# Performance work log

Hardware: AMD Instinct MI355X
Metric: run time of the kernel (lower is better)

Reference implementation:

```python
import jax, jax.numpy as jnp
import numpy as np

# Model hyperparameters (match init_kwargs)
DIM = 512
NUM_HEAD = 8
WS = 2
ALPHA = 0.5
HEAD_DIM = DIM // NUM_HEAD            # 64
L_HEAD = int(NUM_HEAD * ALPHA)        # 4
L_DIM = L_HEAD * HEAD_DIM             # 256
H_HEAD = NUM_HEAD - L_HEAD            # 4
H_DIM = H_HEAD * HEAD_DIM             # 256
SCALE = HEAD_DIM ** (-0.5)


def conv1x1(x, W, b):
    # S_conv treated as pointwise 1x1 conv: channel projection
    return jnp.einsum('bchw,oc->bohw', x, W) + b[None, :, None, None]


def setup_inputs() -> dict:
    key = jax.random.key(0)
    ks = jax.random.split(key, 12)
    s = 0.05  # keep attention logits in a sane range
    B, H, W = 8, 64, 64
    return {
        'x':       jax.random.normal(ks[0], (B, DIM, H, W), jnp.float32),
        'W_hqkv':  jax.random.normal(ks[1], (3 * H_DIM, DIM), jnp.float32) * s,
        'b_hqkv':  jax.random.normal(ks[2], (3 * H_DIM,), jnp.float32) * s,
        'W_hproj': jax.random.normal(ks[3], (H_DIM, H_DIM), jnp.float32) * s,
        'b_hproj': jax.random.normal(ks[4], (H_DIM,), jnp.float32) * s,
        'W_lq':    jax.random.normal(ks[5], (L_DIM, DIM), jnp.float32) * s,
        'b_lq':    jax.random.normal(ks[6], (L_DIM,), jnp.float32) * s,
        'W_lkv':   jax.random.normal(ks[7], (2 * L_DIM, DIM), jnp.float32) * s,
        'b_lkv':   jax.random.normal(ks[8], (2 * L_DIM,), jnp.float32) * s,
        'W_lproj': jax.random.normal(ks[9], (L_DIM, L_DIM), jnp.float32) * s,
        'b_lproj': jax.random.normal(ks[10], (L_DIM,), jnp.float32) * s,
    }


def _hifi(x, W_hqkv, b_hqkv, W_hproj, b_hproj):
    B, C, H, W = x.shape
    hg, wg = H // WS, W // WS
    G = hg * wg
    # Faithful to torch: flatten H*W row-major, split into groups of ws*ws
    qkv = conv1x1(x, W_hqkv, b_hqkv).reshape(B, 3, H_HEAD, HEAD_DIM, G, WS * WS)
    qkv = jnp.transpose(qkv, (1, 0, 4, 2, 5, 3))  # (3, B, G, heads, ws2, hd)
    q, k, v = qkv[0], qkv[1], qkv[2]
    attn = jax.nn.softmax(jnp.einsum('bgnid,bgnjd->bgnij', q, k) * SCALE, axis=-1)
    out = jnp.einsum('bgnij,bgnjd->bgnid', attn, v)  # (B, G, heads, ws2, hd)
    out = jnp.transpose(out, (0, 1, 3, 2, 4)).reshape(B, hg, wg, WS, WS, H_DIM)
    out = jnp.transpose(out, (0, 1, 3, 2, 4, 5)).reshape(B, H, W, H_DIM)
    out = jnp.transpose(out, (0, 3, 1, 2))
    return conv1x1(out, W_hproj, b_hproj)


def _lofi(x, W_lq, b_lq, W_lkv, b_lkv, W_lproj, b_lproj):
    B, C, H, W = x.shape
    N = H * W
    q = conv1x1(x, W_lq, b_lq).reshape(B, L_HEAD, HEAD_DIM, N)
    q = jnp.transpose(q, (0, 1, 3, 2))  # (B, heads, N, hd)
    # AvgPool2d(ws, ws)
    x_ = x.reshape(B, C, H // WS, WS, W // WS, WS).mean(axis=(3, 5))
    kv = conv1x1(x_, W_lkv, b_lkv).reshape(B, 2, L_HEAD, HEAD_DIM, -1)
    kv = jnp.transpose(kv, (1, 0, 2, 4, 3))  # (2, B, heads, M, hd)
    k, v = kv[0], kv[1]
    attn = jax.nn.softmax(jnp.einsum('bhnd,bhmd->bhnm', q, k) * SCALE, axis=-1)
    out = jnp.einsum('bhnm,bhmd->bhnd', attn, v)  # (B, heads, N, hd)
    out = jnp.transpose(out, (0, 2, 1, 3)).reshape(B, H, W, L_DIM)
    out = jnp.transpose(out, (0, 3, 1, 2))
    return conv1x1(out, W_lproj, b_lproj)


def reference(x, W_hqkv, b_hqkv, W_hproj, b_hproj, W_lq, b_lq, W_lkv, b_lkv, W_lproj, b_lproj):
    x_h = _hifi(x, W_hqkv, b_hqkv, W_hproj, b_hproj)
    x_l = _lofi(x, W_lq, b_lq, W_lkv, b_lkv, W_lproj, b_lproj)
    return jnp.concatenate([x_h, x_l], axis=1)
```

## Files before the change

kernel.cpp:

```cpp
#include <hip/hip_runtime.h>


typedef __attribute__((ext_vector_type(8))) short bf16x8;
typedef __attribute__((ext_vector_type(4))) float f32x4;
typedef __attribute__((ext_vector_type(4))) unsigned short us4;
typedef __attribute__((ext_vector_type(4))) unsigned int u32x4;

static __device__ __forceinline__ float bf2f(unsigned short u){
  unsigned int x = ((unsigned int)u) << 16; float f; __builtin_memcpy(&f, &x, 4); return f;
}
static __device__ __forceinline__ unsigned short f2bf(float f){
  unsigned int x; __builtin_memcpy(&x, &f, 4);
  x += 0x7fffu + ((x >> 16) & 1u);
  return (unsigned short)(x >> 16);
}

static __device__ __forceinline__ void gload_lds16(const void* g, void* l){
  __builtin_amdgcn_global_load_lds(
      (const __attribute__((address_space(1))) unsigned int*)g,
      (__attribute__((address_space(3))) unsigned int*)l,
      16, 0, 0);
}

static __device__ __forceinline__ int swz(int row, int colu){
  return row*64 + (colu ^ ((row & 7) << 3));
}

__global__ void cvt_weights(const float* __restrict__ w0, const float* __restrict__ w1,
                            const float* __restrict__ w2, const float* __restrict__ w3,
                            const float* __restrict__ w4,
                            unsigned short* __restrict__ d0, unsigned short* __restrict__ d1,
                            unsigned short* __restrict__ d2, unsigned short* __restrict__ d3,
                            unsigned short* __restrict__ d4)
{
  int i = (int)(blockIdx.x*256 + threadIdx.x);
  const float* src; unsigned short* dst; int j;
  if      (i < 98304) { src = w0; dst = d0; j = i; }
  else if (i < 131072){ src = w1; dst = d1; j = i - 98304; }
  else if (i < 196608){ src = w2; dst = d2; j = i - 131072; }
  else if (i < 212992){ src = w3; dst = d3; j = i - 196608; }
  else                { src = w4; dst = d4; j = i - 212992; }
  f32x4 v = *(const f32x4*)(src + (long)j*4);
  us4 o;
  #pragma unroll
  for (int q = 0; q < 4; q++) o[q] = f2bf(v[q]);
  *(us4*)(dst + (long)j*4) = o;
}

template<int BM,int BN,int WM,int WN,bool OUT_T,bool OUT_F32>
__global__ __launch_bounds__(WM*WN*64)
void gemm_bt(const unsigned short* __restrict__ A, const unsigned short* __restrict__ B,
             const float* __restrict__ bias, void* __restrict__ Cv,
             int K, int lda, int ldb, int ldc,
             int NB, int z0,
             long sAb, long sAn, long sAz,
             long sBb, long sBn, long sBz,
             long sCb, long sCn, long sCz,
             float oscale)
{
  constexpr int NW = WM*WN;
  __shared__ __attribute__((aligned(16))) unsigned short lA[BM*32];
  __shared__ __attribute__((aligned(16))) unsigned short lB[BN*32];
  const int tid  = threadIdx.x;
  const int lane = tid & 63;
  const int wave = tid >> 6;
  const int wm = wave / WN, wn = wave % WN;
  const int zz = z0 + (int)blockIdx.z;
  const int zb = zz / NB, zn = zz % NB;
  const unsigned short* Ab = A + zb*sAb + zn*sAn + (long)blockIdx.z*sAz + (long)blockIdx.x*BM*lda;
  const unsigned short* Bb = B + zb*sBb + zn*sBn + (long)blockIdx.z*sBz + (long)blockIdx.y*BN*ldb;
  const long cOff = zb*sCb + zn*sCn + (long)blockIdx.z*sCz;

  const int srow = wave*16 + (lane >> 2);
  const int scol = (lane & 3) * 8;

  f32x4 acc[4][4] = {};
  const int kq = (lane >> 4) * 8;
  const int lr = lane & 15;
  for (int k0 = 0; k0 < K; k0 += 32){
    if (k0) __syncthreads();
    #pragma unroll
    for (int i = 0; i < BM/(NW*16); i++)
      gload_lds16(Ab + (long)(i*NW*16 + srow)*lda + k0 + scol,
                  &lA[(i*NW*16 + wave*16)*32]);
    #pragma unroll
    for (int i = 0; i < BN/(NW*16); i++)
      gload_lds16(Bb + (long)(i*NW*16 + srow)*ldb + k0 + scol,
                  &lB[(i*NW*16 + wave*16)*32]);
    __syncthreads();
    bf16x8 af[4], bfr[4];
    #pragma unroll
    for (int i = 0; i < 4; i++)
      af[i]  = *(const bf16x8*)(&lA[(wm*64 + i*16 + lr)*32 + kq]);
    #pragma unroll
    for (int j = 0; j < 4; j++)
      bfr[j] = *(const bf16x8*)(&lB[(wn*64 + j*16 + lr)*32 + kq]);
    #pragma unroll
    for (int i = 0; i < 4; i++)
      #pragma unroll
      for (int j = 0; j < 4; j++)
        acc[i][j] = __builtin_amdgcn_mfma_f32_16x16x32_bf16(af[i], bfr[j], acc[i][j], 0, 0, 0);
  }
  const int row0 = (int)blockIdx.x*BM + wm*64;
  const int col0 = (int)blockIdx.y*BN + wn*64;
  #pragma unroll
  for (int j = 0; j < 4; j++){
    const int c = col0 + j*16 + (lane & 15);
    const float bv = bias ? bias[c] : 0.f;
    #pragma unroll
    for (int i = 0; i < 4; i++){
      const int r = row0 + i*16 + ((lane >> 4) << 2);
      f32x4 v = acc[i][j];
      if (OUT_T && OUT_F32){
        float* Cf = (float*)Cv + cOff;
        f32x4 w;
        #pragma unroll
        for (int q = 0; q < 4; q++) w[q] = (v[q] + bv) * oscale;
        *(f32x4*)(Cf + (long)c*ldc + r) = w;
      } else {
        unsigned short* Cb = (unsigned short*)Cv + cOff;
        #pragma unroll
        for (int q = 0; q < 4; q++) Cb[(long)(r + q)*ldc + c] = f2bf((v[q] + bv) * oscale);
      }
    }
  }
}

__global__ __launch_bounds__(256)
void hifi_fused(const unsigned short* __restrict__ xT,
                const unsigned short* __restrict__ W,
                const float* __restrict__ bias,
                unsigned short* __restrict__ attnh)
{
  __shared__ __attribute__((aligned(16))) unsigned short lA[128*32];
  __shared__ __attribute__((aligned(16))) unsigned short lB[192*32];
  const int tid  = threadIdx.x;
  const int lane = tid & 63;
  const int wave = tid >> 6;
  const int lr = lane & 15;
  const int lg = lane >> 4;
  const int n  = (int)blockIdx.y;
  const long bz = (long)blockIdx.z;
  const unsigned short* Ab = xT + (bz*4096 + (long)blockIdx.x*128)*512;

  const int srow = wave*16 + (lane >> 2);
  const int scol = (lane & 3) * 8;
  const int kq = lg * 8;

  f32x4 acc[2][12] = {};
  for (int k0 = 0; k0 < 512; k0 += 32){
    if (k0) __syncthreads();
    #pragma unroll
    for (int i = 0; i < 2; i++)
      gload_lds16(Ab + (long)(i*64 + srow)*512 + k0 + scol,
                  &lA[(i*64 + wave*16)*32]);
    #pragma unroll
    for (int i = 0; i < 3; i++)
      gload_lds16(W + (long)(i*256 + n*64 + srow)*512 + k0 + scol,
                  &lB[(i*64 + wave*16)*32]);
    __syncthreads();
    bf16x8 af[2];
    #pragma unroll
    for (int mi = 0; mi < 2; mi++)
      af[mi] = *(const bf16x8*)(&lA[(wave*32 + mi*16 + lr)*32 + kq]);
    #pragma unroll
    for (int j = 0; j < 12; j++){
      bf16x8 bfr = *(const bf16x8*)(&lB[(j*16 + lr)*32 + kq]);
      #pragma unroll
      for (int mi = 0; mi < 2; mi++)
        acc[mi][j] = __builtin_amdgcn_mfma_f32_16x16x32_bf16(af[mi], bfr, acc[mi][j], 0, 0, 0);
    }
  }
  float bq[4], bk[4], bv[4];
  #pragma unroll
  for (int j = 0; j < 4; j++){
    bq[j] = bias[      n*64 + j*16 + lr];
    bk[j] = bias[256 + n*64 + j*16 + lr];
    bv[j] = bias[512 + n*64 + j*16 + lr];
  }
  unsigned short* Ob = attnh + bz*4096*256 + n*64;
  #pragma unroll
  for (int mi = 0; mi < 2; mi++){
    float qa[4][4], ka[4][4], va[4][4];
    #pragma unroll
    for (int j = 0; j < 4; j++)
      #pragma unroll
      for (int t = 0; t < 4; t++){
        qa[j][t] = acc[mi][j][t]   + bq[j];
        ka[j][t] = acc[mi][4+j][t] + bk[j];
        va[j][t] = acc[mi][8+j][t] + bv[j];
      }
    float S[4][4];
    #pragma unroll
    for (int t = 0; t < 4; t++)
      #pragma unroll
      for (int u = 0; u < 4; u++){
        float s = qa[0][t]*ka[0][u];
        s += qa[1][t]*ka[1][u];
        s += qa[2][t]*ka[2][u];
        s += qa[3][t]*ka[3][u];
        s += __shfl_xor(s, 1); s += __shfl_xor(s, 2);
        s += __shfl_xor(s, 4); s += __shfl_xor(s, 8);
        S[t][u] = s;
      }
    const int g  = (int)blockIdx.x*32 + wave*8 + mi*4 + lg;
    const int gh = g >> 5, gw = g & 31;
    #pragma unroll
    for (int t = 0; t < 4; t++){
      float m = fmaxf(fmaxf(S[t][0], S[t][1]), fmaxf(S[t][2], S[t][3]));
      float e0 = exp2f((S[t][0]-m)*0.1803368801f);
      float e1 = exp2f((S[t][1]-m)*0.1803368801f);
      float e2 = exp2f((S[t][2]-m)*0.1803368801f);
      float e3 = exp2f((S[t][3]-m)*0.1803368801f);
      float inv = 1.f / ((e0+e1) + (e2+e3));
      int pp = (2*gh + (t >> 1))*64 + 2*gw + (t & 1);
      unsigned short* orow = Ob + (long)pp*256;
      #pragma unroll
      for (int j = 0; j < 4; j++){
        float o = (e0*va[j][0] + e1*va[j][1] + e2*va[j][2] + e3*va[j][3]) * inv;
        orow[j*16 + lr] = f2bf(o);
      }
    }
  }
}

__global__ void transpose_xT(const float* __restrict__ x, unsigned short* __restrict__ xT)
{
  __shared__ __attribute__((aligned(16))) unsigned short t[64][72];
  const int tid = threadIdx.x;
  const int b = blockIdx.z, ct = blockIdx.y, pt = blockIdx.x;
  const long c0 = (long)ct*64, p0 = (long)pt*64;
  const float* src = x + ((long)b*512 + c0)*4096 + p0;
  for (int s = tid; s < 1024; s += 256){
    int cl = s >> 4, seg = s & 15;
    f32x4 v = *(const f32x4*)(src + (long)cl*4096 + seg*4);
    us4 o;
    #pragma unroll
    for (int q = 0; q < 4; q++) o[q] = f2bf(v[q]);
    *(us4*)(&t[cl][seg*4]) = o;
  }
  __syncthreads();
  unsigned short* dst = xT + ((long)b*4096 + p0)*512 + c0;
  for (int s = tid; s < 512; s += 256){
    int pl = s >> 3, seg = s & 7;
    unsigned short w[8];
    #pragma unroll
    for (int q = 0; q < 8; q++) w[q] = t[seg*8 + q][pl];
    *(bf16x8*)(dst + (long)pl*512 + seg*8) = *(bf16x8*)w;
  }
}

__global__ void pool_xT(const unsigned short* __restrict__ xT, unsigned short* __restrict__ xp)
{
  long idx = (long)blockIdx.x*256 + threadIdx.x;
  int cseg = (int)(idx & 63);
  int m    = (int)((idx >> 6) & 1023);
  int b    = (int)(idx >> 16);
  int gh = m >> 5, gw = m & 31;
  long p = (long)(gh*2)*64 + gw*2;
  const unsigned short* src = xT + ((long)b*4096 + p)*512 + cseg*8;
  bf16x8 r0 = *(const bf16x8*)(src);
  bf16x8 r1 = *(const bf16x8*)(src + 512);
  bf16x8 r2 = *(const bf16x8*)(src + 64*512);
  bf16x8 r3 = *(const bf16x8*)(src + 65*512);
  unsigned short o[8];
  #pragma unroll
  for (int q = 0; q < 8; q++)
    o[q] = f2bf((bf2f((unsigned short)r0[q]) + bf2f((unsigned short)r1[q]) +
                 bf2f((unsigned short)r2[q]) + bf2f((unsigned short)r3[q])) * 0.25f);
  *(bf16x8*)(xp + ((long)b*1024 + m)*512 + cseg*8) = *(bf16x8*)o;
}

__global__ void transpose_vT(const unsigned short* __restrict__ lkv, unsigned short* __restrict__ vT)
{
  __shared__ __attribute__((aligned(16))) unsigned short t[64][72];
  const int tid = threadIdx.x;
  const int pair = blockIdx.y;
  const int b = pair >> 2, n = pair & 3;
  const long m0 = (long)blockIdx.x*64;
  const unsigned short* src = lkv + ((long)b*1024 + m0)*512 + 256 + n*64;
  for (int s = tid; s < 512; s += 256){
    int ml = s >> 3, seg = s & 7;
    bf16x8 v = *(const bf16x8*)(src + (long)ml*512 + seg*8);
    *(bf16x8*)(&t[ml][seg*8]) = v;
  }
  __syncthreads();
  unsigned short* dst = vT + (long)pair*64*1024 + m0;
  for (int s = tid; s < 512; s += 256){
    int dl = s >> 3, seg = s & 7;
    unsigned short w[8];
    #pragma unroll
    for (int q = 0; q < 8; q++){
      int c = seg*8 + q;
      int kvi = ((c >> 5) & 1)*16 + ((c >> 2) & 1)*32 + ((c >> 3) & 3)*4 + (c & 3);
      w[q] = t[kvi][dl];
    }
    *(bf16x8*)(dst + (long)dl*1024 + seg*8) = *(bf16x8*)w;
  }
}

__global__ __launch_bounds__(256, 3)
void lofi_flash(const unsigned short* __restrict__ lq,
                const unsigned short* __restrict__ lkv,
                const unsigned short* __restrict__ vT,
                unsigned short* __restrict__ attnl)
{
  __shared__ __attribute__((aligned(16))) unsigned short Klds[2][64*64];
  __shared__ __attribute__((aligned(16))) unsigned short Vlds[2][64*64];
  const int tid  = threadIdx.x;
  const int lane = tid & 63;
  const int wave = tid >> 6;
  const int pair = blockIdx.y;
  const int b = pair >> 2, n = pair & 3;
  const int wq0 = (int)blockIdx.x*128 + wave*32;
  const int lr = lane & 15;
  const int lg = lane >> 4;

  const unsigned short* Qbase = lq + ((long)b*4096 + wq0)*256 + n*64;
  bf16x8 qf[2][2];
  #pragma unroll
  for (int mi = 0; mi < 2; mi++)
    #pragma unroll
    for (int kk = 0; kk < 2; kk++)
      qf[mi][kk] = *(const bf16x8*)(Qbase + (long)(mi*16 + lr)*256 + kk*32 + lg*8);

  f32x4 Oacc[2][4] = {};
  float psum[2] = {};

  const unsigned short* Kg = lkv + (long)b*1024*512 + n*64;
  const unsigned short* Vg = vT + (long)pair*64*1024;

  const int rK = tid >> 3;
  const int sg = (tid & 7) * 8;
  bf16x8 k0, k1, v0, v1;
  k0 = *(const bf16x8*)(Kg + (long)rK*512 + sg);
  k1 = *(const bf16x8*)(Kg + (long)(rK + 32)*512 + sg);
  v0 = *(const bf16x8*)(Vg + (long)rK*1024 + sg);
  v1 = *(const bf16x8*)(Vg + (long)(rK + 32)*1024 + sg);
  *(bf16x8*)(&Klds[0][swz(rK, sg)])      = k0;
  *(bf16x8*)(&Klds[0][swz(rK + 32, sg)]) = k1;
  *(bf16x8*)(&Vlds[0][swz(rK, sg)])      = v0;
  *(bf16x8*)(&Vlds[0][swz(rK + 32, sg)]) = v1;
  __syncthreads();

  for (int t = 0; t < 16; t++){
    const int p = t & 1;
    if (t < 15){
      const int kv1 = (t + 1)*64;
      k0 = *(const bf16x8*)(Kg + (long)(kv1 + rK)*512 + sg);
      k1 = *(const bf16x8*)(Kg + (long)(kv1 + rK + 32)*512 + sg);
      v0 = *(const bf16x8*)(Vg + (long)rK*1024 + kv1 + sg);
      v1 = *(const bf16x8*)(Vg + (long)(rK + 32)*1024 + kv1 + sg);
    }
    f32x4 S[4][2] = {};
    bf16x8 kf[4][2];
    #pragma unroll
    for (int nj = 0; nj < 4; nj++)
      #pragma unroll
      for (int kk = 0; kk < 2; kk++)
        kf[nj][kk] = *(const bf16x8*)(&Klds[p][swz(nj*16 + lr, kk*32 + lg*8)]);
    __builtin_amdgcn_s_setprio(1);
    #pragma unroll
    for (int nj = 0; nj < 4; nj++)
      #pragma unroll
      for (int mi = 0; mi < 2; mi++)
        #pragma unroll
        for (int kk = 0; kk < 2; kk++)
          S[nj][mi] = __builtin_amdgcn_mfma_f32_16x16x32_bf16(kf[nj][kk], qf[mi][kk], S[nj][mi], 0, 0, 0);
    __builtin_amdgcn_s_setprio(0);
    bf16x8 pf[2][2];
    #pragma unroll
    for (int mi = 0; mi < 2; mi++){
      float ps = 0.f;
      u32x4 a0, a1;
      #pragma unroll
      for (int nj = 0; nj < 4; nj++){
        float e0 = exp2f(S[nj][mi][0]);
        float e1 = exp2f(S[nj][mi][1]);
        float e2 = exp2f(S[nj][mi][2]);
        float e3 = exp2f(S[nj][mi][3]);
        ps += (e0 + e1) + (e2 + e3);
        unsigned int lo, hi;
        asm("v_cvt_pk_bf16_f32 %0, %1, %2" : "=v"(lo) : "v"(e0), "v"(e1));
        asm("v_cvt_pk_bf16_f32 %0, %1, %2" : "=v"(hi) : "v"(e2), "v"(e3));
        if (nj == 0){ a0[0] = lo; a0[1] = hi; }
        else if (nj == 1){ a1[0] = lo; a1[1] = hi; }
        else if (nj == 2){ a0[2] = lo; a0[3] = hi; }
        else { a1[2] = lo; a1[3] = hi; }
      }
      psum[mi] += ps;
      __builtin_memcpy(&pf[mi][0], &a0, 16);
      __builtin_memcpy(&pf[mi][1], &a1, 16);
    }
    bf16x8 vf[4][2];
    #pragma unroll
    for (int dj = 0; dj < 4; dj++)
      #pragma unroll
      for (int kk = 0; kk < 2; kk++)
        vf[dj][kk] = *(const bf16x8*)(&Vlds[p][swz(dj*16 + lr, kk*32 + lg*8)]);
    __builtin_amdgcn_s_setprio(1);
    #pragma unroll
    for (int mi = 0; mi < 2; mi++)
      #pragma unroll
      for (int dj = 0; dj < 4; dj++)
        #pragma unroll
        for (int kk = 0; kk < 2; kk++)
          Oacc[mi][dj] = __builtin_amdgcn_mfma_f32_16x16x32_bf16(pf[mi][kk], vf[dj][kk], Oacc[mi][dj], 0, 0, 0);
    __builtin_amdgcn_s_setprio(0);
    if (t < 15){
      *(bf16x8*)(&Klds[p^1][swz(rK, sg)])      = k0;
      *(bf16x8*)(&Klds[p^1][swz(rK + 32, sg)]) = k1;
      *(bf16x8*)(&Vlds[p^1][swz(rK, sg)])      = v0;
      *(bf16x8*)(&Vlds[p^1][swz(rK + 32, sg)]) = v1;
    }
    __syncthreads();
  }
  #pragma unroll
  for (int mi = 0; mi < 2; mi++){
    float s = psum[mi];
    s += __shfl_xor(s, 16);
    s += __shfl_xor(s, 32);
    psum[mi] = s;
  }
  unsigned short* Ob = attnl + ((long)b*4096 + wq0)*256 + n*64;
  #pragma unroll
  for (int mi = 0; mi < 2; mi++)
    #pragma unroll
    for (int rg = 0; rg < 4; rg++){
      float l = __shfl(psum[mi], lg*4 + rg);
      float inv = 1.f / l;
      int r = mi*16 + lg*4 + rg;
      #pragma unroll
      for (int dj = 0; dj < 4; dj++)
        Ob[(long)r*256 + dj*16 + lr] = f2bf(Oacc[mi][dj][rg] * inv);
    }
}

extern "C" void kernel_launch(void* const* d_in, const int* in_sizes, int n_in,
                              void* d_out, int out_size, void* d_ws, size_t ws_size,
                              hipStream_t stream)
{
  (void)in_sizes; (void)n_in; (void)out_size;
  const float* x      = (const float*)d_in[0];
  const float* Whqkv  = (const float*)d_in[1];
  const float* bhqkv  = (const float*)d_in[2];
  const float* Whproj = (const float*)d_in[3];
  const float* bhproj = (const float*)d_in[4];
  const float* Wlq    = (const float*)d_in[5];
  const float* blq    = (const float*)d_in[6];
  const float* Wlkv   = (const float*)d_in[7];
  const float* blkv   = (const float*)d_in[8];
  const float* Wlproj = (const float*)d_in[9];
  const float* blproj = (const float*)d_in[10];
  float* out = (float*)d_out;
  char* ws = (char*)d_ws;

  if (ws_size < 73138176u) return;
  unsigned short* xT      = (unsigned short*)(ws + 0);
  unsigned short* attnl   = (unsigned short*)(ws + 0);
  unsigned short* attnh8  = (unsigned short*)(ws + 33554432L);
  unsigned short* lqb     = (unsigned short*)(ws + 33554432L);
  unsigned short* xp      = (unsigned short*)(ws + 50331648L);
  unsigned short* lkvb    = (unsigned short*)(ws + 58720256L);
  unsigned short* vTb     = (unsigned short*)(ws + 67108864L);
  unsigned short* Whqkv_b = (unsigned short*)(ws + 71303168L);
  unsigned short* Wlq_b   = (unsigned short*)(ws + 72089600L);
  unsigned short* Wlkv_b  = (unsigned short*)(ws + 72351744L);
  unsigned short* Whproj_b= (unsigned short*)(ws + 72876032L);
  unsigned short* Wlproj_b= (unsigned short*)(ws + 73007104L);

  cvt_weights<<<896, 256, 0, stream>>>(Whqkv, Wlq, Wlkv, Whproj, Wlproj,
                                       Whqkv_b, Wlq_b, Wlkv_b, Whproj_b, Wlproj_b);

  transpose_xT<<<dim3(64,8,8),256,0,stream>>>(x, xT);

  hifi_fused<<<dim3(32,4,8),256,0,stream>>>(xT, Whqkv_b, bhqkv, attnh8);

  gemm_bt<128,128,2,2,true,true><<<dim3(32,2,8),256,0,stream>>>(attnh8, Whproj_b, bhproj,
      out,
      256, 256, 256, 4096, 1, 0,
      0, 0, 4096L*256,   0, 0, 0,   0, 0, 512L*4096,  1.0f);

  gemm_bt<128,128,2,2,false,false><<<dim3(32,2,8),256,0,stream>>>(xT, Wlq_b, blq, lqb,
      512, 512, 512, 256, 1, 0,
      4096L*512, 0, 0,   0, 0, 0,   4096L*256, 0, 0,  0.1803368801f);
  pool_xT<<<2048,256,0,stream>>>(xT, xp);
  gemm_bt<128,128,2,2,false,false><<<dim3(8,4,8),256,0,stream>>>(xp, Wlkv_b, blkv, lkvb,
      512, 512, 512, 512, 1, 0,
      1024L*512, 0, 0,   0, 0, 0,   1024L*512, 0, 0,  1.0f);
  transpose_vT<<<dim3(16,32),256,0,stream>>>(lkvb, vTb);
  lofi_flash<<<dim3(32,32),256,0,stream>>>(lqb, lkvb, vTb, attnl);
  gemm_bt<128,128,2,2,true,true><<<dim3(32,2,8),256,0,stream>>>(attnl, Wlproj_b, blproj,
      out + 256L*4096,
      256, 256, 256, 4096, 1, 0,
      4096L*256, 0, 0,   0, 0, 0,   512L*4096, 0, 0,  1.0f);
}
```

Baseline: 190.0 us.

## Fuse pooling into transpose and lofi Q projection into hifi QKV kernel

Folds the 2x2 average pool into the x transpose kernel so pooled rows are computed from the LDS tile, which removes a separate pass over xT. The lofi Q projection is merged into the hifi QKV GEMM by loading Wlq as a fourth 64-column B tile, so xT is read once for both. The hifi kernel now uses 64-row tiles, and hifi plus its output projection run in two batch chunks so the attention intermediate fits in a smaller workspace that stays cache-resident. The costs are more launches and smaller per-block M tiles, which give less A reuse.

```diff
diff --git a/kernel.cpp b/kernel.cpp
--- a/kernel.cpp
+++ b/kernel.cpp
@@ -5,6 +5,8 @@
 typedef __attribute__((ext_vector_type(4))) float f32x4;
 typedef __attribute__((ext_vector_type(4))) unsigned short us4;
 typedef __attribute__((ext_vector_type(4))) unsigned int u32x4;
+
+#define LQ_SCALE 0.1803368801f
 
 static __device__ __forceinline__ float bf2f(unsigned short u){
   unsigned int x = ((unsigned int)u) << 16; float f; __builtin_memcpy(&f, &x, 4); return f;
@@ -126,14 +128,58 @@
   }
 }
 
+__global__ void transpose_pool_xT(const float* __restrict__ x,
+                                  unsigned short* __restrict__ xT,
+                                  unsigned short* __restrict__ xp)
+{
+  __shared__ __attribute__((aligned(16))) unsigned short t[2][64][72];
+  const int tid = threadIdx.x;
+  const int b = blockIdx.z, ct = blockIdx.y, pt2 = blockIdx.x;
+  const long c0 = (long)ct*64;
+  const int y0 = pt2*2;
+  const float* src = x + ((long)b*512 + c0)*4096 + (long)y0*64;
+  for (int s = tid; s < 2048; s += 256){
+    int tile = s >> 10, cl = (s >> 4) & 63, seg = s & 15;
+    f32x4 v = *(const f32x4*)(src + (long)cl*4096 + tile*64 + seg*4);
+    us4 o;
+    #pragma unroll
+    for (int q = 0; q < 4; q++) o[q] = f2bf(v[q]);
+    *(us4*)(&t[tile][cl][seg*4]) = o;
+  }
+  __syncthreads();
+  unsigned short* dst = xT + ((long)b*4096 + (long)y0*64)*512 + c0;
+  for (int s = tid; s < 1024; s += 256){
+    int tile = s >> 9, pl = (s >> 3) & 63, seg = s & 7;
+    unsigned short w[8];
+    #pragma unroll
+    for (int q = 0; q < 8; q++) w[q] = t[tile][seg*8 + q][pl];
+    *(bf16x8*)(dst + ((long)tile*64 + pl)*512 + seg*8) = *(bf16x8*)w;
+  }
+  {
+    int gx = tid >> 3, seg = tid & 7;
+    unsigned short o[8];
+    #pragma unroll
+    for (int q = 0; q < 8; q++){
+      int cc = seg*8 + q;
+      float s = bf2f(t[0][cc][2*gx]) + bf2f(t[0][cc][2*gx + 1]) +
+                bf2f(t[1][cc][2*gx]) + bf2f(t[1][cc][2*gx + 1]);
+      o[q] = f2bf(s * 0.25f);
+    }
+    *(bf16x8*)(xp + ((long)b*1024 + pt2*32 + gx)*512 + c0 + seg*8) = *(bf16x8*)o;
+  }
+}
+
 __global__ __launch_bounds__(256)
 void hifi_fused(const unsigned short* __restrict__ xT,
                 const unsigned short* __restrict__ W,
+                const unsigned short* __restrict__ Wlq,
                 const float* __restrict__ bias,
-                unsigned short* __restrict__ attnh)
-{
-  __shared__ __attribute__((aligned(16))) unsigned short lA[128*32];
-  __shared__ __attribute__((aligned(16))) unsigned short lB[192*32];
+                const float* __restrict__ blq,
+                unsigned short* __restrict__ attnh,
+                unsigned short* __restrict__ lqb)
+{
+  __shared__ __attribute__((aligned(16))) unsigned short lA[64*32];
+  __shared__ __attribute__((aligned(16))) unsigned short lB[256*32];
   const int tid  = threadIdx.x;
   const int lane = tid & 63;
   const int wave = tid >> 6;
@@ -141,134 +187,86 @@
   const int lg = lane >> 4;
   const int n  = (int)blockIdx.y;
   const long bz = (long)blockIdx.z;
-  const unsigned short* Ab = xT + (bz*4096 + (long)blockIdx.x*128)*512;
+  const unsigned short* Ab = xT + (bz*4096 + (long)blockIdx.x*64)*512;
 
   const int srow = wave*16 + (lane >> 2);
   const int scol = (lane & 3) * 8;
   const int kq = lg * 8;
 
-  f32x4 acc[2][12] = {};
+  f32x4 acc[16] = {};
   for (int k0 = 0; k0 < 512; k0 += 32){
     if (k0) __syncthreads();
-    #pragma unroll
-    for (int i = 0; i < 2; i++)
-      gload_lds16(Ab + (long)(i*64 + srow)*512 + k0 + scol,
-                  &lA[(i*64 + wave*16)*32]);
+    gload_lds16(Ab + (long)srow*512 + k0 + scol, &lA[(wave*16)*32]);
     #pragma unroll
     for (int i = 0; i < 3; i++)
       gload_lds16(W + (long)(i*256 + n*64 + srow)*512 + k0 + scol,
                   &lB[(i*64 + wave*16)*32]);
+    gload_lds16(Wlq + (long)(n*64 + srow)*512 + k0 + scol,
+                &lB[(192 + wave*16)*32]);
     __syncthreads();
-    bf16x8 af[2];
-    #pragma unroll
-    for (int mi = 0; mi < 2; mi++)
-      af[mi] = *(const bf16x8*)(&lA[(wave*32 + mi*16 + lr)*32 + kq]);
-    #pragma unroll
-    for (int j = 0; j < 12; j++){
+    bf16x8 af = *(const bf16x8*)(&lA[(wave*16 + lr)*32 + kq]);
+    #pragma unroll
+    for (int j = 0; j < 16; j++){
       bf16x8 bfr = *(const bf16x8*)(&lB[(j*16 + lr)*32 + kq]);
-      #pragma unroll
-      for (int mi = 0; mi < 2; mi++)
-        acc[mi][j] = __builtin_amdgcn_mfma_f32_16x16x32_bf16(af[mi], bfr, acc[mi][j], 0, 0, 0);
-    }
-  }
-  float bq[4], bk[4], bv[4];
+      acc[j] = __builtin_amdgcn_mfma_f32_16x16x32_bf16(af, bfr, acc[j], 0, 0, 0);
+    }
+  }
+  const int row0 = (int)blockIdx.x*64 + wave*16 + lg*4;
+  {
+    unsigned short* Lb = lqb + (bz*4096 + row0)*256 + n*64;
+    #pragma unroll
+    for (int j = 0; j < 4; j++){
+      float bv = blq[n*64 + j*16 + lr];
+      #pragma unroll
+      for (int t = 0; t < 4; t++)
+        Lb[(long)t*256 + j*16 + lr] = f2bf((acc[12 + j][t] + bv) * LQ_SCALE);
+    }
+  }
+  float qa[4][4], ka[4][4], va[4][4];
   #pragma unroll
   for (int j = 0; j < 4; j++){
-    bq[j] = bias[      n*64 + j*16 + lr];
-    bk[j] = bias[256 + n*64 + j*16 + lr];
-    bv[j] = bias[512 + n*64 + j*16 + lr];
-  }
+    float bq = bias[      n*64 + j*16 + lr];
+    float bk = bias[256 + n*64 + j*16 + lr];
+    float bv = bias[512 + n*64 + j*16 + lr];
+    #pragma unroll
+    for (int t = 0; t < 4; t++){
+      qa[j][t] = acc[j][t]     + bq;
+      ka[j][t] = acc[4 + j][t] + bk;
+      va[j][t] = acc[8 + j][t] + bv;
+    }
+  }
+  float S[4][4];
+  #pragma unroll
+  for (int t = 0; t < 4; t++)
+    #pragma unroll
+    for (int u = 0; u < 4; u++){
+      float s = qa[0][t]*ka[0][u];
+      s += qa[1][t]*ka[1][u];
+      s += qa[2][t]*ka[2][u];
+      s += qa[3][t]*ka[3][u];
+      s += __shfl_xor(s, 1); s += __shfl_xor(s, 2);
+      s += __shfl_xor(s, 4); s += __shfl_xor(s, 8);
+      S[t][u] = s;
+    }
+  const int g  = (int)blockIdx.x*16 + wave*4 + lg;
+  const int gh = g >> 5, gw = g & 31;
   unsigned short* Ob = attnh + bz*4096*256 + n*64;
   #pragma unroll
-  for (int mi = 0; mi < 2; mi++){
-    float qa[4][4], ka[4][4], va[4][4];
-    #pragma unroll
-    for (int j = 0; j < 4; j++)
-      #pragma unroll
-      for (int t = 0; t < 4; t++){
-        qa[j][t] = acc[mi][j][t]   + bq[j];
-        ka[j][t] = acc[mi][4+j][t] + bk[j];
-        va[j][t] = acc[mi][8+j][t] + bv[j];
-      }
-    float S[4][4];
-    #pragma unroll
-    for (int t = 0; t < 4; t++)
-      #pragma unroll
-      for (int u = 0; u < 4; u++){
-        float s = qa[0][t]*ka[0][u];
-        s += qa[1][t]*ka[1][u];
-        s += qa[2][t]*ka[2][u];
-        s += qa[3][t]*ka[3][u];
-        s += __shfl_xor(s, 1); s += __shfl_xor(s, 2);
-        s += __shfl_xor(s, 4); s += __shfl_xor(s, 8);
-        S[t][u] = s;
-      }
-    const int g  = (int)blockIdx.x*32 + wave*8 + mi*4 + lg;
-    const int gh = g >> 5, gw = g & 31;
-    #pragma unroll
-    for (int t = 0; t < 4; t++){
-      float m = fmaxf(fmaxf(S[t][0], S[t][1]), fmaxf(S[t][2], S[t][3]));
-      float e0 = exp2f((S[t][0]-m)*0.1803368801f);
-      float e1 = exp2f((S[t][1]-m)*0.1803368801f);
-      float e2 = exp2f((S[t][2]-m)*0.1803368801f);
-      float e3 = exp2f((S[t][3]-m)*0.1803368801f);
-      float inv = 1.f / ((e0+e1) + (e2+e3));
-      int pp = (2*gh + (t >> 1))*64 + 2*gw + (t & 1);
-      unsigned short* orow = Ob + (long)pp*256;
-      #pragma unroll
-      for (int j = 0; j < 4; j++){
-        float o = (e0*va[j][0] + e1*va[j][1] + e2*va[j][2] + e3*va[j][3]) * inv;
-        orow[j*16 + lr] = f2bf(o);
-      }
-    }
-  }
-}
-
-__global__ void transpose_xT(const float* __restrict__ x, unsigned short* __restrict__ xT)
-{
-  __shared__ __attribute__((aligned(16))) unsigned short t[64][72];
-  const int tid = threadIdx.x;
-  const int b = blockIdx.z, ct = blockIdx.y, pt = blockIdx.x;
-  const long c0 = (long)ct*64, p0 = (long)pt*64;
-  const float* src = x + ((long)b*512 + c0)*4096 + p0;
-  for (int s = tid; s < 1024; s += 256){
-    int cl = s >> 4, seg = s & 15;
-    f32x4 v = *(const f32x4*)(src + (long)cl*4096 + seg*4);
-    us4 o;
-    #pragma unroll
-    for (int q = 0; q < 4; q++) o[q] = f2bf(v[q]);
-    *(us4*)(&t[cl][seg*4]) = o;
-  }
-  __syncthreads();
-  unsigned short* dst = xT + ((long)b*4096 + p0)*512 + c0;
-  for (int s = tid; s < 512; s += 256){
-    int pl = s >> 3, seg = s & 7;
-    unsigned short w[8];
-    #pragma unroll
-    for (int q = 0; q < 8; q++) w[q] = t[seg*8 + q][pl];
-    *(bf16x8*)(dst + (long)pl*512 + seg*8) = *(bf16x8*)w;
-  }
-}
-
-__global__ void pool_xT(const unsigned short* __restrict__ xT, unsigned short* __restrict__ xp)
-{
-  long idx = (long)blockIdx.x*256 + threadIdx.x;
-  int cseg = (int)(idx & 63);
-  int m    = (int)((idx >> 6) & 1023);
-  int b    = (int)(idx >> 16);
-  int gh = m >> 5, gw = m & 31;
-  long p = (long)(gh*2)*64 + gw*2;
-  const unsigned short* src = xT + ((long)b*4096 + p)*512 + cseg*8;
-  bf16x8 r0 = *(const bf16x8*)(src);
-  bf16x8 r1 = *(const bf16x8*)(src + 512);
-  bf16x8 r2 = *(const bf16x8*)(src + 64*512);
-  bf16x8 r3 = *(const bf16x8*)(src + 65*512);
-  unsigned short o[8];
-  #pragma unroll
-  for (int q = 0; q < 8; q++)
-    o[q] = f2bf((bf2f((unsigned short)r0[q]) + bf2f((unsigned short)r1[q]) +
-                 bf2f((unsigned short)r2[q]) + bf2f((unsigned short)r3[q])) * 0.25f);
-  *(bf16x8*)(xp + ((long)b*1024 + m)*512 + cseg*8) = *(bf16x8*)o;
+  for (int t = 0; t < 4; t++){
+    float m = fmaxf(fmaxf(S[t][0], S[t][1]), fmaxf(S[t][2], S[t][3]));
+    float e0 = exp2f((S[t][0]-m)*LQ_SCALE);
+    float e1 = exp2f((S[t][1]-m)*LQ_SCALE);
+    float e2 = exp2f((S[t][2]-m)*LQ_SCALE);
+    float e3 = exp2f((S[t][3]-m)*LQ_SCALE);
+    float inv = 1.f / ((e0+e1) + (e2+e3));
+    int pp = (2*gh + (t >> 1))*64 + 2*gw + (t & 1);
+    unsigned short* orow = Ob + (long)pp*256;
+    #pragma unroll
+    for (int j = 0; j < 4; j++){
+      float o = (e0*va[j][0] + e1*va[j][1] + e2*va[j][2] + e3*va[j][3]) * inv;
+      orow[j*16 + lr] = f2bf(o);
+    }
+  }
 }
 
 __global__ void transpose_vT(const unsigned short* __restrict__ lkv, unsigned short* __restrict__ vT)
@@ -455,36 +453,36 @@
   float* out = (float*)d_out;
   char* ws = (char*)d_ws;
 
-  if (ws_size < 73138176u) return;
+  if (ws_size < 68943872u) return;
   unsigned short* xT      = (unsigned short*)(ws + 0);
   unsigned short* attnl   = (unsigned short*)(ws + 0);
-  unsigned short* attnh8  = (unsigned short*)(ws + 33554432L);
   unsigned short* lqb     = (unsigned short*)(ws + 33554432L);
   unsigned short* xp      = (unsigned short*)(ws + 50331648L);
+  unsigned short* vTb     = (unsigned short*)(ws + 50331648L);
+  unsigned short* attnh_c = (unsigned short*)(ws + 58720256L);
   unsigned short* lkvb    = (unsigned short*)(ws + 58720256L);
-  unsigned short* vTb     = (unsigned short*)(ws + 67108864L);
-  unsigned short* Whqkv_b = (unsigned short*)(ws + 71303168L);
-  unsigned short* Wlq_b   = (unsigned short*)(ws + 72089600L);
-  unsigned short* Wlkv_b  = (unsigned short*)(ws + 72351744L);
-  unsigned short* Whproj_b= (unsigned short*)(ws + 72876032L);
-  unsigned short* Wlproj_b= (unsigned short*)(ws + 73007104L);
+  unsigned short* Whqkv_b = (unsigned short*)(ws + 67108864L);
+  unsigned short* Wlq_b   = (unsigned short*)(ws + 67895296L);
+  unsigned short* Wlkv_b  = (unsigned short*)(ws + 68157440L);
+  unsigned short* Whproj_b= (unsigned short*)(ws + 68681728L);
+  unsigned short* Wlproj_b= (unsigned short*)(ws + 68812800L);
 
   cvt_weights<<<896, 256, 0, stream>>>(Whqkv, Wlq, Wlkv, Whproj, Wlproj,
                                        Whqkv_b, Wlq_b, Wlkv_b, Whproj_b, Wlproj_b);
 
-  transpose_xT<<<dim3(64,8,8),256,0,stream>>>(x, xT);
-
-  hifi_fused<<<dim3(32,4,8),256,0,stream>>>(xT, Whqkv_b, bhqkv, attnh8);
-
-  gemm_bt<128,128,2,2,true,true><<<dim3(32,2,8),256,0,stream>>>(attnh8, Whproj_b, bhproj,
-      out,
-      256, 256, 256, 4096, 1, 0,
-      0, 0, 4096L*256,   0, 0, 0,   0, 0, 512L*4096,  1.0f);
-
-  gemm_bt<128,128,2,2,false,false><<<dim3(32,2,8),256,0,stream>>>(xT, Wlq_b, blq, lqb,
-      512, 512, 512, 256, 1, 0,
-      4096L*512, 0, 0,   0, 0, 0,   4096L*256, 0, 0,  0.1803368801f);
-  pool_xT<<<2048,256,0,stream>>>(xT, xp);
+  transpose_pool_xT<<<dim3(32,8,8),256,0,stream>>>(x, xT, xp);
+
+  for (int c = 0; c < 2; c++){
+    const unsigned short* xTc = xT + (long)c*4*4096*512;
+    unsigned short* lqc = lqb + (long)c*4*4096*256;
+    hifi_fused<<<dim3(64,4,4),256,0,stream>>>(xTc, Whqkv_b, Wlq_b, bhqkv, blq,
+                                              attnh_c, lqc);
+    gemm_bt<128,128,2,2,true,true><<<dim3(32,2,4),256,0,stream>>>(attnh_c, Whproj_b, bhproj,
+        out + (long)c*4*512*4096,
+        256, 256, 256, 4096, 1, 0,
+        0, 0, 4096L*256,   0, 0, 0,   0, 0, 512L*4096,  1.0f);
+  }
+
   gemm_bt<128,128,2,2,false,false><<<dim3(8,4,8),256,0,stream>>>(xp, Wlkv_b, blkv, lkvb,
       512, 512, 512, 512, 1, 0,
       1024L*512, 0, 0,   0, 0, 0,   1024L*512, 0, 0,  1.0f);
```

After: 211.1 us. 1.11x slower.
